# Kernel optimization log

Measured on AMD Instinct MI355X. Metric: run time of the kernel, lower is better.

## Reference

```python
import jax, jax.numpy as jnp
import numpy as np

D_MODEL = 1024
N_HEADS = 16
D_HEAD = D_MODEL // N_HEADS


def setup_inputs() -> dict:
    key = jax.random.key(0)
    ks = jax.random.split(key, 5)
    s_in = 1.0 / np.sqrt(D_MODEL)
    x = jax.random.normal(ks[0], (4, 2048, D_MODEL), dtype=jnp.float32)
    W_qkv = jax.random.uniform(ks[1], (D_MODEL, 3 * D_MODEL), jnp.float32, -s_in, s_in)
    b_qkv = jax.random.uniform(ks[2], (3 * D_MODEL,), jnp.float32, -s_in, s_in)
    W_out = jax.random.uniform(ks[3], (D_MODEL, D_MODEL), jnp.float32, -s_in, s_in)
    b_out = jax.random.uniform(ks[4], (D_MODEL,), jnp.float32, -s_in, s_in)
    return {"x": x, "W_qkv": W_qkv, "b_qkv": b_qkv, "W_out": W_out, "b_out": b_out}


def reference(x, W_qkv, b_qkv, W_out, b_out):
    B, T, C = x.shape
    qkv = x @ W_qkv + b_qkv                       # [B,T,3C]
    q, k, v = jnp.split(qkv, 3, axis=-1)
    # [B,T,C] -> [B,H,T,Dh]
    def heads(t):
        return t.reshape(B, T, N_HEADS, D_HEAD).transpose(0, 2, 1, 3)
    q, k, v = heads(q), heads(k), heads(v)
    scale = 1.0 / np.sqrt(D_HEAD).astype(np.float32)
    attn = jnp.einsum('bhqd,bhkd->bhqk', q, k) * scale   # [B,H,T,T]
    causal = jnp.tril(jnp.ones((T, T), dtype=bool))
    attn = jnp.where(causal, attn, -jnp.inf)
    attn_weights = jax.nn.softmax(attn, axis=-1)
    out = jnp.einsum('bhqk,bhkd->bhqd', attn_weights, v)  # [B,H,T,Dh]
    out = out.transpose(0, 2, 1, 3).reshape(B, T, C)
    return out @ W_out + b_out
```

## Files before the change

### kernel.cpp

```cpp
#include <hip/hip_runtime.h>
#include <hip/hip_bf16.h>

#define BATCH   4
#define SEQ     2048
#define DMODEL  1024
#define NHEADS  16
#define DHEAD   64
#define MROWS   (BATCH*SEQ)
#define QKV_N   (3*DMODEL)
#define NEG_BIG (-1.0e30f)
#define WS_NEED ((size_t)MROWS * 2*DMODEL * sizeof(__hip_bfloat16))
#define SCALE_Q 0.18033688011112042f

using bf16 = __hip_bfloat16;
typedef __attribute__((ext_vector_type(8))) short short8;
typedef __attribute__((ext_vector_type(4))) float floatx4;

__device__ __align__(16) unsigned short g_wqT[QKV_N * DMODEL];
__device__ __align__(16) unsigned short g_woT[DMODEL * DMODEL];
__device__ __align__(16) unsigned short g_xb [MROWS * DMODEL];

__device__ __forceinline__ unsigned short f2bf_rne(float f) {
    union { bf16 b; unsigned short u; } t;
    t.b = __float2bfloat16(f);
    return t.u;
}

__device__ __forceinline__ void gload_lds16(const void* g, void* l) {
    __builtin_amdgcn_global_load_lds(
        (const __attribute__((address_space(1))) unsigned*)g,
        (__attribute__((address_space(3))) unsigned*)l, 16, 0, 0);
}

__global__ __launch_bounds__(256) void cast_x(const float* __restrict__ x) {
    const size_t i = ((size_t)blockIdx.x*256 + threadIdx.x)*8;
    const float4 a = *(const float4*)(x + i);
    const float4 b = *(const float4*)(x + i + 4);
    union { uint4 u4; unsigned short us[8]; } o;
    o.us[0]=f2bf_rne(a.x); o.us[1]=f2bf_rne(a.y); o.us[2]=f2bf_rne(a.z); o.us[3]=f2bf_rne(a.w);
    o.us[4]=f2bf_rne(b.x); o.us[5]=f2bf_rne(b.y); o.us[6]=f2bf_rne(b.z); o.us[7]=f2bf_rne(b.w);
    *(uint4*)(g_xb + i) = o.u4;
}

__global__ __launch_bounds__(256) void transcast_w(
    const float* __restrict__ W, int N, int which)
{
    unsigned short* dst = which ? g_woT : g_wqT;
    __shared__ unsigned short T[64][72];
    const int n0 = blockIdx.x * 64, k0 = blockIdx.y * 64;
    const int tid = threadIdx.x;
    const int r = tid >> 2, c0 = (tid & 3) * 16;

#pragma unroll
    for (int it = 0; it < 4; ++it) {
        const float4 v = *(const float4*)(W + (size_t)(k0 + r)*N + n0 + c0 + it*4);
        T[r][c0 + it*4 + 0] = f2bf_rne(v.x);
        T[r][c0 + it*4 + 1] = f2bf_rne(v.y);
        T[r][c0 + it*4 + 2] = f2bf_rne(v.z);
        T[r][c0 + it*4 + 3] = f2bf_rne(v.w);
    }
    __syncthreads();
    const int nr = tid >> 2, kc0 = (tid & 3) * 16;
#pragma unroll
    for (int it = 0; it < 2; ++it) {
        union { uint4 u4; unsigned short us[8]; } o;
#pragma unroll
        for (int j = 0; j < 8; j++) o.us[j] = T[kc0 + it*8 + j][nr];
        *(uint4*)(dst + (size_t)(n0 + nr)*DMODEL + k0 + kc0 + it*8) = o.u4;
    }
}

template<int QKV_MODE>
__global__ __launch_bounds__(256) void gemm_mfma(
    const void* __restrict__ Av, const float* __restrict__ bias,
    void* __restrict__ C0, void* __restrict__ C1, void* __restrict__ C2)
{
    const unsigned short* A  = QKV_MODE ? g_xb : (const unsigned short*)Av;
    const unsigned short* BT = QKV_MODE ? g_wqT : g_woT;
    __shared__ alignas(16) unsigned short As[128*32];
    __shared__ alignas(16) unsigned short Bs[128*32];

    const int tid = threadIdx.x;
    const int bm = blockIdx.y, bn = blockIdx.x;
    const int w = tid >> 6, lane = tid & 63;
    const int m16 = lane & 15, quad = lane >> 4;
    const int m0 = (w & 1) * 64, n0w = (w >> 1) * 64;

    const int lrow  = lane >> 2;
    const int lcol  = (lane & 3) * 8;
    const unsigned short* aG = A  + (size_t)(bm*128 + w*32 + lrow)*DMODEL + lcol;
    const unsigned short* bG = BT + (size_t)(bn*128 + w*32 + lrow)*DMODEL + lcol;
    char* asL = (char*)As + w*2048;
    char* bsL = (char*)Bs + w*2048;

    floatx4 acc[4][4];
#pragma unroll
    for (int i = 0; i < 4; i++)
#pragma unroll
        for (int j = 0; j < 4; j++) { acc[i][j][0]=0.f; acc[i][j][1]=0.f; acc[i][j][2]=0.f; acc[i][j][3]=0.f; }

    for (int k0 = 0; k0 < DMODEL; k0 += 32) {
        __syncthreads();
        gload_lds16(aG + k0,              asL);
        gload_lds16(aG + 16*DMODEL + k0,  asL + 1024);
        gload_lds16(bG + k0,              bsL);
        gload_lds16(bG + 16*DMODEL + k0,  bsL + 1024);
        __syncthreads();

        short8 af[4], bf4[4];
#pragma unroll
        for (int i = 0; i < 4; ++i) af[i]  = *(const short8*)&As[(m0 + i*16 + m16)*32 + quad*8];
#pragma unroll
        for (int j = 0; j < 4; ++j) bf4[j] = *(const short8*)&Bs[(n0w + j*16 + m16)*32 + quad*8];
#pragma unroll
        for (int i = 0; i < 4; ++i)
#pragma unroll
            for (int j = 0; j < 4; ++j)
                acc[i][j] = __builtin_amdgcn_mfma_f32_16x16x32_bf16(af[i], bf4[j], acc[i][j], 0, 0, 0);
    }

    const int gcolb = bn*128;
    float bv[4];
#pragma unroll
    for (int j = 0; j < 4; ++j) bv[j] = bias[gcolb + n0w + j*16 + m16];

    if (QKV_MODE) {
        const int seg = gcolb >> 10;
        if (seg < 2) {
            bf16* Cout = (bf16*)(seg ? C1 : C0);
            const float sc = seg ? 1.0f : SCALE_Q;
#pragma unroll
            for (int i = 0; i < 4; ++i)
#pragma unroll
                for (int r = 0; r < 4; ++r) {
                    const int gm = bm*128 + m0 + i*16 + quad*4 + r;
#pragma unroll
                    for (int j = 0; j < 4; ++j) {
                        const int cc = (gcolb + n0w + j*16 + m16) & 1023;
                        Cout[(size_t)gm*DMODEL + cc] = __float2bfloat16((acc[i][j][r] + bv[j]) * sc);
                    }
                }
        } else {
            bf16* VT = (bf16*)C2;
#pragma unroll
            for (int i = 0; i < 4; ++i) {
                const int gm0 = bm*128 + m0 + i*16 + quad*4;
                const int bb = gm0 >> 11, t0 = gm0 & 2047;
#pragma unroll
                for (int j = 0; j < 4; ++j) {
                    const int cv = (gcolb & 1023) + n0w + j*16 + m16;
                    const int hh = cv >> 6, dd = cv & 63;
                    union { unsigned long long u8; unsigned short us[4]; } o;
#pragma unroll
                    for (int r = 0; r < 4; ++r) o.us[r] = f2bf_rne(acc[i][j][r] + bv[j]);
                    *(unsigned long long*)(VT + ((size_t)((bb*NHEADS + hh)*DHEAD + dd))*SEQ + t0) = o.u8;
                }
            }
        }
    } else {
        float* Cout = (float*)C0;
#pragma unroll
        for (int i = 0; i < 4; ++i)
#pragma unroll
            for (int r = 0; r < 4; ++r) {
                const int gm = bm*128 + m0 + i*16 + quad*4 + r;
#pragma unroll
                for (int j = 0; j < 4; ++j) {
                    const int cc = (gcolb + n0w + j*16 + m16) & 1023;
                    Cout[(size_t)gm*DMODEL + cc] = acc[i][j][r] + bv[j];
                }
            }
    }
}

__global__ __launch_bounds__(256, 2) void attn_mfma3(
    const bf16* __restrict__ Qg, const bf16* __restrict__ Kg,
    const bf16* __restrict__ VTg, bf16* __restrict__ Og)
{
    __shared__ alignas(16) unsigned short Kt[2][64][72];
    __shared__ alignas(16) unsigned short Vt[2][64][72];
    __shared__ alignas(16) unsigned short Ps[4][32][72];

    const int x = blockIdx.x;
    const int b = x >> 7, h = (x >> 3) & 15, p = x & 7;
    const int tid = threadIdx.x;
    const int w = tid >> 6, lane = tid & 63;
    const int m16 = lane & 15, quad = lane >> 4;
    const int sr = tid >> 2, sc0 = (tid & 3) * 8;
    const size_t bh = (size_t)(b*NHEADS + h);

    for (int seg = 0; seg < 2; ++seg) {
        const int qt  = seg ? (15 - p) : p;
        const int nkt = 2*qt + 2;
        const int qrow0 = qt*128 + w*32;

        short8 qf[2][2];
#pragma unroll
        for (int i = 0; i < 2; ++i)
#pragma unroll
            for (int c = 0; c < 2; ++c)
                qf[i][c] = *(const short8*)(Qg + (size_t)(b*SEQ + qrow0 + i*16 + m16)*DMODEL
                                            + h*DHEAD + c*32 + quad*8);

        floatx4 of[2][4];
        float mrow[2], lrow[2];
#pragma unroll
        for (int i = 0; i < 2; ++i) {
            mrow[i] = NEG_BIG; lrow[i] = 0.f;
#pragma unroll
            for (int nt = 0; nt < 4; ++nt) { of[i][nt][0]=0.f; of[i][nt][1]=0.f; of[i][nt][2]=0.f; of[i][nt][3]=0.f; }
        }

        {
            const bf16* kp = Kg  + (size_t)(b*SEQ + sr)*DMODEL + h*DHEAD + sc0;
            const bf16* vp = VTg + (bh*DHEAD + sr)*SEQ + sc0;
            const uint4 a0 = *(const uint4*)kp, a1 = *(const uint4*)(kp + 32);
            const uint4 b0 = *(const uint4*)vp, b1 = *(const uint4*)(vp + 32);
            __syncthreads();
            *(uint4*)&Kt[0][sr][sc0]      = a0;
            *(uint4*)&Kt[0][sr][sc0 + 32] = a1;
            *(uint4*)&Vt[0][sr][sc0]      = b0;
            *(uint4*)&Vt[0][sr][sc0 + 32] = b1;
            __syncthreads();
        }

        for (int kt = 0; kt < nkt; ++kt) {
            const int buf = kt & 1;
            const int k064 = kt * 64;
            const bool pre = (kt + 1 < nkt);
            uint4 kr0, kr1, vr0, vr1;
            if (pre) {
                const bf16* kp = Kg  + (size_t)(b*SEQ + k064 + 64 + sr)*DMODEL + h*DHEAD + sc0;
                const bf16* vp = VTg + (bh*DHEAD + sr)*SEQ + k064 + 64 + sc0;
                kr0 = *(const uint4*)kp; kr1 = *(const uint4*)(kp + 32);
                vr0 = *(const uint4*)vp; vr1 = *(const uint4*)(vp + 32);
            }

            floatx4 sf[2][4];
#pragma unroll
            for (int t4 = 0; t4 < 4; ++t4) {
                const short8 kf0 = *(const short8*)&Kt[buf][t4*16 + m16][quad*8];
                const short8 kf1 = *(const short8*)&Kt[buf][t4*16 + m16][32 + quad*8];
#pragma unroll
                for (int i = 0; i < 2; ++i) {
                    floatx4 a; a[0]=0.f; a[1]=0.f; a[2]=0.f; a[3]=0.f;
                    a = __builtin_amdgcn_mfma_f32_16x16x32_bf16(kf0, qf[i][0], a, 0, 0, 0);
                    a = __builtin_amdgcn_mfma_f32_16x16x32_bf16(kf1, qf[i][1], a, 0, 0, 0);
                    sf[i][t4] = a;
                }
            }

            const bool need_mask = (k064 + 63 > qrow0);
#pragma unroll
            for (int i = 0; i < 2; ++i) {
                if (need_mask) {
                    const int qg = qrow0 + i*16 + m16;
#pragma unroll
                    for (int t4 = 0; t4 < 4; ++t4)
#pragma unroll
                        for (int r = 0; r < 4; ++r)
                            if (k064 + t4*16 + quad*4 + r > qg) sf[i][t4][r] = NEG_BIG;
                }
                float mx = sf[i][0][0];
#pragma unroll
                for (int t4 = 0; t4 < 4; ++t4)
#pragma unroll
                    for (int r = 0; r < 4; ++r) mx = fmaxf(mx, sf[i][t4][r]);
                mx = fmaxf(mx, __shfl_xor(mx, 16));
                mx = fmaxf(mx, __shfl_xor(mx, 32));

                const float mnew  = fmaxf(mrow[i], mx);
                const float alpha = exp2f(mrow[i] - mnew);
                mrow[i] = mnew;

                float rs = 0.f;
#pragma unroll
                for (int t4 = 0; t4 < 4; ++t4) {
#pragma unroll
                    for (int r = 0; r < 4; ++r) {
                        const float pv = exp2f(sf[i][t4][r] - mnew);
                        sf[i][t4][r] = pv;
                        rs += pv;
                    }
                }
                rs += __shfl_xor(rs, 16);
                rs += __shfl_xor(rs, 32);
                lrow[i] = lrow[i]*alpha + rs;
#pragma unroll
                for (int nt = 0; nt < 4; ++nt)
#pragma unroll
                    for (int r = 0; r < 4; ++r) of[i][nt][r] *= alpha;

#pragma unroll
                for (int t4 = 0; t4 < 4; ++t4) {
                    union { unsigned long long u8; unsigned short us[4]; } o;
#pragma unroll
                    for (int r = 0; r < 4; ++r) o.us[r] = f2bf_rne(sf[i][t4][r]);
                    *(unsigned long long*)&Ps[w][i*16 + m16][t4*16 + quad*4] = o.u8;
                }
            }

            short8 pf[2][2];
#pragma unroll
            for (int i = 0; i < 2; ++i)
#pragma unroll
                for (int c = 0; c < 2; ++c)
                    pf[i][c] = *(const short8*)&Ps[w][i*16 + m16][c*32 + quad*8];
#pragma unroll
            for (int nt = 0; nt < 4; ++nt) {
                const short8 vf0 = *(const short8*)&Vt[buf][nt*16 + m16][quad*8];
                const short8 vf1 = *(const short8*)&Vt[buf][nt*16 + m16][32 + quad*8];
#pragma unroll
                for (int i = 0; i < 2; ++i) {
                    of[i][nt] = __builtin_amdgcn_mfma_f32_16x16x32_bf16(vf0, pf[i][0], of[i][nt], 0, 0, 0);
                    of[i][nt] = __builtin_amdgcn_mfma_f32_16x16x32_bf16(vf1, pf[i][1], of[i][nt], 0, 0, 0);
                }
            }

            if (pre) {
                *(uint4*)&Kt[buf^1][sr][sc0]      = kr0;
                *(uint4*)&Kt[buf^1][sr][sc0 + 32] = kr1;
                *(uint4*)&Vt[buf^1][sr][sc0]      = vr0;
                *(uint4*)&Vt[buf^1][sr][sc0 + 32] = vr1;
            }
            __syncthreads();
        }

#pragma unroll
        for (int i = 0; i < 2; ++i) {
            const float rl = 1.f / fmaxf(lrow[i], 1e-20f);
            const size_t rowbase = (size_t)(b*SEQ + qrow0 + i*16 + m16)*DMODEL + h*DHEAD;
#pragma unroll
            for (int nt = 0; nt < 4; ++nt) {
                union { unsigned long long u8; unsigned short us[4]; } o;
#pragma unroll
                for (int r = 0; r < 4; ++r) o.us[r] = f2bf_rne(of[i][nt][r] * rl);
                *(unsigned long long*)(Og + rowbase + nt*16 + quad*4) = o.u8;
            }
        }
    }
}

__global__ void diag_fill(float* out, int n, float val) {
    int i = blockIdx.x*blockDim.x + threadIdx.x;
    if (i < n) out[i] = val;
}

extern "C" void kernel_launch(void* const* d_in, const int* in_sizes, int n_in,
                              void* d_out, int out_size, void* d_ws, size_t ws_size,
                              hipStream_t stream) {
    const float* x     = (const float*)d_in[0];
    const float* W_qkv = (const float*)d_in[1];
    const float* b_qkv = (const float*)d_in[2];
    const float* W_out = (const float*)d_in[3];
    const float* b_out = (const float*)d_in[4];

    if (ws_size < WS_NEED) {
        const float val = 100.f + (float)(ws_size >> 20);
        diag_fill<<<(out_size + 255)/256, 256, 0, stream>>>((float*)d_out, out_size, val);
        return;
    }

    bf16* Qb  = (bf16*)d_out;
    bf16* VTb = (bf16*)d_out + (size_t)MROWS*DMODEL;
    bf16* Kb  = (bf16*)d_ws;
    bf16* Ob  = (bf16*)d_ws + (size_t)MROWS*DMODEL;

    cast_x<<<MROWS*DMODEL/2048, 256, 0, stream>>>(x);
    {
        dim3 gq(QKV_N/64, DMODEL/64);
        transcast_w<<<gq, 256, 0, stream>>>(W_qkv, QKV_N, 0);
        dim3 go(DMODEL/64, DMODEL/64);
        transcast_w<<<go, 256, 0, stream>>>(W_out, DMODEL, 1);
    }
    {
        dim3 g(QKV_N/128, MROWS/128);
        gemm_mfma<1><<<g, 256, 0, stream>>>(nullptr, b_qkv, Qb, Kb, VTb);
    }
    {
        attn_mfma3<<<512, 256, 0, stream>>>(Qb, Kb, VTb, Ob);
    }
    {
        dim3 g(DMODEL/128, MROWS/128);
        gemm_mfma<0><<<g, 256, 0, stream>>>(Ob, b_out, d_out, nullptr, nullptr);
    }
}
```

Before: 306.4 us.

## Replace 128x128 GEMM with double-buffered 256x256 tile kernel using swizzled LDS

Both projection GEMMs now use a 512-thread kernel with 256x256 output tiles and a K-step of 64. A 128KB LDS double buffer lets the next tile's global-to-LDS loads overlap the current tile's MFMAs, with partial vmcnt waits in place of full syncs. The LDS layout is XOR-swizzled to avoid bank conflicts, and s_setprio raises priority around the MFMA bursts. The aim is higher operand reuse and less load stall per MFMA. In exchange the grids shrink to 384 and 128 blocks, which can leave CUs idle or unevenly loaded, and the large LDS use limits occupancy.

```diff
diff --git a/kernel.cpp b/kernel.cpp
--- a/kernel.cpp
+++ b/kernel.cpp
@@ -71,105 +71,183 @@
 }
 
 template<int QKV_MODE>
-__global__ __launch_bounds__(256) void gemm_mfma(
+__global__ __launch_bounds__(512, 2) void gemm256(
     const void* __restrict__ Av, const float* __restrict__ bias,
     void* __restrict__ C0, void* __restrict__ C1, void* __restrict__ C2)
 {
-    const unsigned short* A  = QKV_MODE ? g_xb : (const unsigned short*)Av;
+    const unsigned short* A  = QKV_MODE ? g_xb  : (const unsigned short*)Av;
     const unsigned short* BT = QKV_MODE ? g_wqT : g_woT;
-    __shared__ alignas(16) unsigned short As[128*32];
-    __shared__ alignas(16) unsigned short Bs[128*32];
-
-    const int tid = threadIdx.x;
-    const int bm = blockIdx.y, bn = blockIdx.x;
-    const int w = tid >> 6, lane = tid & 63;
-    const int m16 = lane & 15, quad = lane >> 4;
-    const int m0 = (w & 1) * 64, n0w = (w >> 1) * 64;
-
-    const int lrow  = lane >> 2;
-    const int lcol  = (lane & 3) * 8;
-    const unsigned short* aG = A  + (size_t)(bm*128 + w*32 + lrow)*DMODEL + lcol;
-    const unsigned short* bG = BT + (size_t)(bn*128 + w*32 + lrow)*DMODEL + lcol;
-    char* asL = (char*)As + w*2048;
-    char* bsL = (char*)Bs + w*2048;
-
-    floatx4 acc[4][4];
-#pragma unroll
-    for (int i = 0; i < 4; i++)
-#pragma unroll
-        for (int j = 0; j < 4; j++) { acc[i][j][0]=0.f; acc[i][j][1]=0.f; acc[i][j][2]=0.f; acc[i][j][3]=0.f; }
-
-    for (int k0 = 0; k0 < DMODEL; k0 += 32) {
-        __syncthreads();
-        gload_lds16(aG + k0,              asL);
-        gload_lds16(aG + 16*DMODEL + k0,  asL + 1024);
-        gload_lds16(bG + k0,              bsL);
-        gload_lds16(bG + 16*DMODEL + k0,  bsL + 1024);
-        __syncthreads();
-
-        short8 af[4], bf4[4];
-#pragma unroll
-        for (int i = 0; i < 4; ++i) af[i]  = *(const short8*)&As[(m0 + i*16 + m16)*32 + quad*8];
-#pragma unroll
-        for (int j = 0; j < 4; ++j) bf4[j] = *(const short8*)&Bs[(n0w + j*16 + m16)*32 + quad*8];
-#pragma unroll
-        for (int i = 0; i < 4; ++i)
+
+    __shared__ __align__(16) char smem[131072];
+    char* const sA = smem;
+    char* const sB = smem + 65536;
+
+    const int tid  = threadIdx.x;
+    const int w    = tid >> 6, lane = tid & 63;
+    const int m16  = lane & 15, quad = lane >> 4;
+    const int rw   = w >> 1, cw = w & 1;
+    const int bm   = blockIdx.y, bn = blockIdx.x;
+
+    const int rL = lane >> 2;
+    const int cD = (lane & 3) ^ ((lane >> 3) & 3);
+    const unsigned short* gA = A  + (size_t)(bm*256 + rL)*DMODEL + cD*8;
+    const unsigned short* gB = BT + (size_t)(bn*256 + rL)*DMODEL + cD*8;
+
+    const int laneRd = m16*64 + (quad ^ ((m16 >> 1) & 3))*16;
+
+    floatx4 acc[4][2][4];
+#pragma unroll
+    for (int q = 0; q < 4; ++q)
+#pragma unroll
+        for (int i = 0; i < 2; ++i)
+#pragma unroll
+            for (int j = 0; j < 4; ++j) {
+                acc[q][i][j][0]=0.f; acc[q][i][j][1]=0.f;
+                acc[q][i][j][2]=0.f; acc[q][i][j][3]=0.f;
+            }
+
+    auto stageA = [&](int buf, int half, int k0) {
+        char* l0 = sA + buf*32768 + half*16384 + w*1024;
+        gload_lds16(gA + (size_t)(half*128 + (w>>1)*16)*DMODEL + k0 + (w&1)*32, l0);
+        gload_lds16(gA + (size_t)(half*128 + ((w>>1)+4)*16)*DMODEL + k0 + (w&1)*32, l0 + 8192);
+    };
+    auto stageB = [&](int buf, int half, int k0) {
+        char* l0 = sB + buf*32768 + half*16384 + w*1024;
+        gload_lds16(gB + (size_t)(half*128 + (w>>1)*16)*DMODEL + k0 + (w&1)*32, l0);
+        gload_lds16(gB + (size_t)(half*128 + ((w>>1)+4)*16)*DMODEL + k0 + (w&1)*32, l0 + 8192);
+    };
+
+    stageA(0, 0, 0); stageB(0, 0, 0); stageA(0, 1, 0); stageB(0, 1, 0);
+    asm volatile("s_waitcnt vmcnt(0)" ::: "memory");
+    __builtin_amdgcn_s_barrier();
+
+    const int NT = DMODEL / 64;
+    for (int t = 0; t < NT; ++t) {
+        const int  buf = t & 1;
+        const int  k1  = (t + 1) * 64;
+        const bool st  = (t + 1 < NT);
+        char* const Abuf = sA + buf*32768;
+        char* const Bbuf = sB + buf*32768;
+
+#pragma unroll
+        for (int q = 0; q < 4; ++q) {
+            const int qm = q >> 1, qn = q & 1;
+
+            short8 af[2][2], bfr[4][2];
+#pragma unroll
+            for (int i = 0; i < 2; ++i)
+#pragma unroll
+                for (int kh = 0; kh < 2; ++kh)
+                    af[i][kh] = *(const short8*)(Abuf + qm*16384
+                                    + ((rw*2 + i)*2 + kh)*1024 + laneRd);
 #pragma unroll
             for (int j = 0; j < 4; ++j)
-                acc[i][j] = __builtin_amdgcn_mfma_f32_16x16x32_bf16(af[i], bf4[j], acc[i][j], 0, 0, 0);
-    }
-
-    const int gcolb = bn*128;
-    float bv[4];
-#pragma unroll
-    for (int j = 0; j < 4; ++j) bv[j] = bias[gcolb + n0w + j*16 + m16];
+#pragma unroll
+                for (int kh = 0; kh < 2; ++kh)
+                    bfr[j][kh] = *(const short8*)(Bbuf + qn*16384
+                                    + ((cw*4 + j)*2 + kh)*1024 + laneRd);
+
+            if (st) {
+                if      (q == 0) stageA(buf^1, 0, k1);
+                else if (q == 1) stageB(buf^1, 0, k1);
+                else if (q == 2) stageA(buf^1, 1, k1);
+                else             stageB(buf^1, 1, k1);
+            }
+
+            __builtin_amdgcn_s_barrier();
+
+            __builtin_amdgcn_s_setprio(1);
+#pragma unroll
+            for (int i = 0; i < 2; ++i)
+#pragma unroll
+                for (int j = 0; j < 4; ++j) {
+                    acc[q][i][j] = __builtin_amdgcn_mfma_f32_16x16x32_bf16(
+                        af[i][0], bfr[j][0], acc[q][i][j], 0, 0, 0);
+                    acc[q][i][j] = __builtin_amdgcn_mfma_f32_16x16x32_bf16(
+                        af[i][1], bfr[j][1], acc[q][i][j], 0, 0, 0);
+                }
+            __builtin_amdgcn_s_setprio(0);
+
+            if (q == 0) {
+                if (st) { asm volatile("s_waitcnt vmcnt(2)" ::: "memory"); }
+                else    { asm volatile("s_waitcnt vmcnt(0)" ::: "memory"); }
+            }
+            if (q == 3) {
+                if (st) { asm volatile("s_waitcnt vmcnt(4)" ::: "memory"); }
+                else    { asm volatile("s_waitcnt vmcnt(0)" ::: "memory"); }
+            }
+            __builtin_amdgcn_s_barrier();
+        }
+    }
+
+    float bv[2][4];
+#pragma unroll
+    for (int qn = 0; qn < 2; ++qn)
+#pragma unroll
+        for (int j = 0; j < 4; ++j)
+            bv[qn][j] = bias[bn*256 + qn*128 + cw*64 + j*16 + m16];
 
     if (QKV_MODE) {
-        const int seg = gcolb >> 10;
+        const int seg = bn >> 2;
         if (seg < 2) {
             bf16* Cout = (bf16*)(seg ? C1 : C0);
             const float sc = seg ? 1.0f : SCALE_Q;
 #pragma unroll
-            for (int i = 0; i < 4; ++i)
-#pragma unroll
-                for (int r = 0; r < 4; ++r) {
-                    const int gm = bm*128 + m0 + i*16 + quad*4 + r;
-#pragma unroll
-                    for (int j = 0; j < 4; ++j) {
-                        const int cc = (gcolb + n0w + j*16 + m16) & 1023;
-                        Cout[(size_t)gm*DMODEL + cc] = __float2bfloat16((acc[i][j][r] + bv[j]) * sc);
+            for (int q = 0; q < 4; ++q) {
+                const int qm = q >> 1, qn = q & 1;
+#pragma unroll
+                for (int i = 0; i < 2; ++i)
+#pragma unroll
+                    for (int r = 0; r < 4; ++r) {
+                        const int gm = bm*256 + qm*128 + rw*32 + i*16 + quad*4 + r;
+#pragma unroll
+                        for (int j = 0; j < 4; ++j) {
+                            const int cc = (bn*256 + qn*128 + cw*64 + j*16 + m16) & 1023;
+                            Cout[(size_t)gm*DMODEL + cc] =
+                                __float2bfloat16((acc[q][i][j][r] + bv[qn][j]) * sc);
+                        }
                     }
-                }
+            }
         } else {
             bf16* VT = (bf16*)C2;
 #pragma unroll
-            for (int i = 0; i < 4; ++i) {
-                const int gm0 = bm*128 + m0 + i*16 + quad*4;
-                const int bb = gm0 >> 11, t0 = gm0 & 2047;
-#pragma unroll
-                for (int j = 0; j < 4; ++j) {
-                    const int cv = (gcolb & 1023) + n0w + j*16 + m16;
-                    const int hh = cv >> 6, dd = cv & 63;
-                    union { unsigned long long u8; unsigned short us[4]; } o;
-#pragma unroll
-                    for (int r = 0; r < 4; ++r) o.us[r] = f2bf_rne(acc[i][j][r] + bv[j]);
-                    *(unsigned long long*)(VT + ((size_t)((bb*NHEADS + hh)*DHEAD + dd))*SEQ + t0) = o.u8;
+            for (int q = 0; q < 4; ++q) {
+                const int qm = q >> 1, qn = q & 1;
+#pragma unroll
+                for (int i = 0; i < 2; ++i) {
+                    const int gm0 = bm*256 + qm*128 + rw*32 + i*16 + quad*4;
+                    const int bb = gm0 >> 11, t0 = gm0 & 2047;
+#pragma unroll
+                    for (int j = 0; j < 4; ++j) {
+                        const int cv = (bn*256 + qn*128 + cw*64 + j*16 + m16) & 1023;
+                        const int hh = cv >> 6, dd = cv & 63;
+                        union { unsigned long long u8; unsigned short us[4]; } o;
+#pragma unroll
+                        for (int r = 0; r < 4; ++r)
+                            o.us[r] = f2bf_rne(acc[q][i][j][r] + bv[qn][j]);
+                        *(unsigned long long*)(VT
+                            + ((size_t)((bb*NHEADS + hh)*DHEAD + dd))*SEQ + t0) = o.u8;
+                    }
                 }
             }
         }
     } else {
         float* Cout = (float*)C0;
 #pragma unroll
-        for (int i = 0; i < 4; ++i)
-#pragma unroll
-            for (int r = 0; r < 4; ++r) {
-                const int gm = bm*128 + m0 + i*16 + quad*4 + r;
-#pragma unroll
-                for (int j = 0; j < 4; ++j) {
-                    const int cc = (gcolb + n0w + j*16 + m16) & 1023;
-                    Cout[(size_t)gm*DMODEL + cc] = acc[i][j][r] + bv[j];
-                }
-            }
+        for (int q = 0; q < 4; ++q) {
+            const int qm = q >> 1, qn = q & 1;
+#pragma unroll
+            for (int i = 0; i < 2; ++i)
+#pragma unroll
+                for (int r = 0; r < 4; ++r) {
+                    const int gm = bm*256 + qm*128 + rw*32 + i*16 + quad*4 + r;
+#pragma unroll
+                    for (int j = 0; j < 4; ++j) {
+                        const int cc = (bn*256 + qn*128 + cw*64 + j*16 + m16) & 1023;
+                        Cout[(size_t)gm*DMODEL + cc] = acc[q][i][j][r] + bv[qn][j];
+                    }
+                }
+        }
     }
 }
 
@@ -374,14 +452,14 @@
         transcast_w<<<go, 256, 0, stream>>>(W_out, DMODEL, 1);
     }
     {
-        dim3 g(QKV_N/128, MROWS/128);
-        gemm_mfma<1><<<g, 256, 0, stream>>>(nullptr, b_qkv, Qb, Kb, VTb);
+        dim3 g(QKV_N/256, MROWS/256);
+        gemm256<1><<<g, 512, 0, stream>>>(nullptr, b_qkv, Qb, Kb, VTb);
     }
     {
         attn_mfma3<<<512, 256, 0, stream>>>(Qb, Kb, VTb, Ob);
     }
     {
-        dim3 g(DMODEL/128, MROWS/128);
-        gemm_mfma<0><<<g, 256, 0, stream>>>(Ob, b_out, d_out, nullptr, nullptr);
-    }
-}
+        dim3 g(DMODEL/256, MROWS/256);
+        gemm256<0><<<g, 512, 0, stream>>>(Ob, b_out, d_out, nullptr, nullptr);
+    }
+}
```

Result: faster. 294.9 us (-3.8%).
